# Kernel tuning notes

Hardware: AMD Instinct MI355X
Metric: run time of the kernel (lower is better)

Reference implementation:

```python
import jax, jax.numpy as jnp
import numpy as np

N_NODES = 50000
N_REL = 500
D = 128
N_EDGES = 600000


def setup_inputs() -> dict:
    key = jax.random.key(0)
    k1, k2, k3, k4, k5 = jax.random.split(key, 5)
    h = jax.random.normal(k1, (N_NODES, D), dtype=jnp.float32)
    g = jax.random.normal(k2, (N_REL, D), dtype=jnp.float32)
    row = jax.random.randint(k3, (N_EDGES,), 0, N_NODES)
    col = jax.random.randint(k4, (N_EDGES,), 0, N_NODES)
    edge_idx = jnp.stack([row, col], axis=0)  # [2, E]
    edge_type = jax.random.randint(k5, (N_EDGES,), 0, N_REL)
    return {"h": h, "g": g, "edge_idx": edge_idx, "edge_type": edge_type}


def reference(h, g, edge_idx, edge_type):
    # d = || h[row] + g[type] - h[col] ||_1 per edge  -> [E]
    row, col = edge_idx[0], edge_idx[1]
    diff = h[row] + g[edge_type] - h[col]  # [E, D] fused gather+combine
    return jnp.sum(jnp.abs(diff), axis=1)
```

## Files before the change

### kernel.cpp

```cpp
#include <hip/hip_runtime.h>
#include <hip/hip_fp16.h>


#define D 128
typedef float f32x2 __attribute__((ext_vector_type(2)));

__global__ void __launch_bounds__(256) KB_cvt(
    const float* __restrict__ h_in, unsigned int* __restrict__ h8, int n4_h,
    const float* __restrict__ g_in, unsigned int* __restrict__ g8, int n4_g)
{
    const int total = n4_h + n4_g;
    for (int i = blockIdx.x * 256 + threadIdx.x; i < total; i += gridDim.x * 256) {
        const bool isH = (i < n4_h);
        const int  j   = isH ? i : i - n4_h;
        const float4 v = isH ? reinterpret_cast<const float4*>(h_in)[j]
                             : reinterpret_cast<const float4*>(g_in)[j];
        unsigned int w = 0;
        w = __builtin_amdgcn_cvt_pk_fp8_f32(v.x, v.y, w, false);
        w = __builtin_amdgcn_cvt_pk_fp8_f32(v.z, v.w, w, true);
        (isH ? h8 : g8)[j] = w;
    }
}

__global__ void __launch_bounds__(256, 4) KB_main(
    const unsigned int* __restrict__ h8,
    const unsigned int* __restrict__ g8,
    const int* __restrict__ eidx,
    const int* __restrict__ etype,
    float* __restrict__ out,
    int E)
{
    const int grp = (blockIdx.x * 256 + (int)threadIdx.x) >> 3;
    const int sub = threadIdx.x & 7;
    const int e0  = grp * 4;
    if (e0 >= E) return;

    int r[4], c[4], t[4];
    #pragma unroll
    for (int k = 0; k < 4; ++k) {
        const int e = min(e0 + k, E - 1);
        r[k] = eidx[e];
        c[k] = eidx[E + e];
        t[k] = etype[e];
    }

    uint4 hr[4], hc[4], gw[4];
    #pragma unroll
    for (int k = 0; k < 4; ++k)
        hr[k] = *reinterpret_cast<const uint4*>(h8 + (size_t)r[k] * 32 + sub * 4);
    #pragma unroll
    for (int k = 0; k < 4; ++k)
        hc[k] = *reinterpret_cast<const uint4*>(h8 + (size_t)c[k] * 32 + sub * 4);
    #pragma unroll
    for (int k = 0; k < 4; ++k)
        gw[k] = *reinterpret_cast<const uint4*>(g8 + (size_t)t[k] * 32 + sub * 4);

    float s0 = 0.f, s1 = 0.f, s2 = 0.f, s3 = 0.f;
    #pragma unroll
    for (int k = 0; k < 4; ++k) {
        const unsigned int ha[4] = {hr[k].x, hr[k].y, hr[k].z, hr[k].w};
        const unsigned int hb[4] = {hc[k].x, hc[k].y, hc[k].z, hc[k].w};
        const unsigned int gg[4] = {gw[k].x, gw[k].y, gw[k].z, gw[k].w};
        float s = 0.f;
        #pragma unroll
        for (int j = 0; j < 4; ++j) {
            const f32x2 a0 = __builtin_amdgcn_cvt_pk_f32_fp8(ha[j], false);
            const f32x2 a1 = __builtin_amdgcn_cvt_pk_f32_fp8(ha[j], true);
            const f32x2 c0 = __builtin_amdgcn_cvt_pk_f32_fp8(hb[j], false);
            const f32x2 c1 = __builtin_amdgcn_cvt_pk_f32_fp8(hb[j], true);
            const f32x2 g0 = __builtin_amdgcn_cvt_pk_f32_fp8(gg[j], false);
            const f32x2 g1 = __builtin_amdgcn_cvt_pk_f32_fp8(gg[j], true);
            s += fabsf(a0.x + g0.x - c0.x) + fabsf(a0.y + g0.y - c0.y)
               + fabsf(a1.x + g1.x - c1.x) + fabsf(a1.y + g1.y - c1.y);
        }
        s += __shfl_xor(s, 4, 8);
        s += __shfl_xor(s, 2, 8);
        s += __shfl_xor(s, 1, 8);
        if (k == 0) s0 = s; else if (k == 1) s1 = s; else if (k == 2) s2 = s; else s3 = s;
    }

    const float v = (sub == 0) ? s0 : (sub == 1) ? s1 : (sub == 2) ? s2 : s3;
    if (sub < 4 && e0 + sub < E) out[e0 + sub] = v;
}

__global__ void __launch_bounds__(256) KB_transe_l1_f32(
    const float* __restrict__ h, const float* __restrict__ g,
    const int* __restrict__ eidx, const int* __restrict__ etype,
    float* __restrict__ out, int E)
{
    const int tid  = blockIdx.x * 256 + threadIdx.x;
    const int edge = tid >> 5;
    const int lane = threadIdx.x & 31;
    if (edge >= E) return;
    const int r = eidx[edge], c = eidx[E + edge], t = etype[edge];
    const int d = lane * 4;
    const float4 hr = *reinterpret_cast<const float4*>(h + (size_t)r * D + d);
    const float4 hc = *reinterpret_cast<const float4*>(h + (size_t)c * D + d);
    const float4 gt = *reinterpret_cast<const float4*>(g + (size_t)t * D + d);
    float s = fabsf(hr.x + gt.x - hc.x) + fabsf(hr.y + gt.y - hc.y)
            + fabsf(hr.z + gt.z - hc.z) + fabsf(hr.w + gt.w - hc.w);
    #pragma unroll
    for (int o = 16; o >= 1; o >>= 1) s += __shfl_xor(s, o, 32);
    if (lane == 0) out[edge] = s;
}

extern "C" void kernel_launch(void* const* d_in, const int* in_sizes, int n_in,
                              void* d_out, int out_size, void* d_ws, size_t ws_size,
                              hipStream_t stream) {
    const float* h     = (const float*)d_in[0];
    const float* g     = (const float*)d_in[1];
    const int*   eidx  = (const int*)d_in[2];
    const int*   etype = (const int*)d_in[3];
    float*       out   = (float*)d_out;

    const int E   = in_sizes[3];
    const int n_h = in_sizes[0];
    const int n_g = in_sizes[1];

    const size_t need = (size_t)n_h + (size_t)n_g;
    const bool ok = (n_h % 4 == 0) && (n_g % 4 == 0) && (n_h % D == 0) && (n_g % D == 0);

    if (ws_size >= need && ok) {
        unsigned int* h8 = (unsigned int*)d_ws;
        unsigned int* g8 = (unsigned int*)((char*)d_ws + (size_t)n_h);
        const int n4_h = n_h / 4, n4_g = n_g / 4;
        const int cgrid = (n4_h + n4_g + 255) / 256;
        KB_cvt<<<cgrid, 256, 0, stream>>>(h, h8, n4_h, g, g8, n4_g);

        const int groups = (E + 3) / 4;
        const long long threads = (long long)groups * 8;
        const int grid = (int)((threads + 255) / 256);
        KB_main<<<grid, 256, 0, stream>>>(h8, g8, eidx, etype, out, E);
    } else {
        const long long threads = (long long)E * 32;
        const int grid = (int)((threads + 255) / 256);
        KB_transe_l1_f32<<<grid, 256, 0, stream>>>(h, g, eidx, etype, out, E);
    }
}
```

Before: 29.33 us.

## Stage relation table in LDS with persistent 1024-thread grid-stride blocks

Copies the fp8 relation embedding table (500x128 bytes, 64KB) into shared memory once per block, and reads relation rows from LDS instead of global memory. The kernel becomes persistent: 512 blocks of 1024 threads loop over 512-edge chunks. This removes one global gather per edge, at the cost of a 64KB LDS footprint that limits occupancy to about one or two blocks per CU, plus an up-front table load in every block.

Result: slower. 31.35 us (+6.9%).

```diff
diff --git a/kernel.cpp b/kernel.cpp
--- a/kernel.cpp
+++ b/kernel.cpp
@@ -3,6 +3,7 @@
 
 
 #define D 128
+#define MAXREL 500
 typedef float f32x2 __attribute__((ext_vector_type(2)));
 
 __global__ void __launch_bounds__(256) KB_cvt(
@@ -22,65 +23,79 @@
     }
 }
 
-__global__ void __launch_bounds__(256, 4) KB_main(
+__global__ void __launch_bounds__(1024) KB_main(
     const unsigned int* __restrict__ h8,
     const unsigned int* __restrict__ g8,
     const int* __restrict__ eidx,
     const int* __restrict__ etype,
     float* __restrict__ out,
-    int E)
+    int E, int ng_u4, int niter)
 {
-    const int grp = (blockIdx.x * 256 + (int)threadIdx.x) >> 3;
+    __shared__ unsigned int gs[MAXREL * (D / 4)];
+
+    {
+        uint4* gsv = reinterpret_cast<uint4*>(gs);
+        const uint4* gv = reinterpret_cast<const uint4*>(g8);
+        for (int i = threadIdx.x; i < ng_u4; i += 1024) gsv[i] = gv[i];
+    }
+    __syncthreads();
+
+    const int grp = threadIdx.x >> 3;
     const int sub = threadIdx.x & 7;
-    const int e0  = grp * 4;
-    if (e0 >= E) return;
 
-    int r[4], c[4], t[4];
-    #pragma unroll
-    for (int k = 0; k < 4; ++k) {
-        const int e = min(e0 + k, E - 1);
-        r[k] = eidx[e];
-        c[k] = eidx[E + e];
-        t[k] = etype[e];
+    for (int it = blockIdx.x; it < niter; it += gridDim.x) {
+        const int e0 = it * 512 + grp * 4;
+        if (e0 >= E) continue;
+
+        int r[4], c[4], t[4];
+        #pragma unroll
+        for (int k = 0; k < 4; ++k) {
+            const int e = min(e0 + k, E - 1);
+            r[k] = eidx[e];
+            c[k] = eidx[E + e];
+            t[k] = etype[e];
+        }
+
+        uint4 hr[4], hc[4];
+        #pragma unroll
+        for (int k = 0; k < 4; ++k)
+            hr[k] = *reinterpret_cast<const uint4*>(h8 + (size_t)r[k] * 32 + sub * 4);
+        #pragma unroll
+        for (int k = 0; k < 4; ++k)
+            hc[k] = *reinterpret_cast<const uint4*>(h8 + (size_t)c[k] * 32 + sub * 4);
+
+        uint4 gw[4];
+        #pragma unroll
+        for (int k = 0; k < 4; ++k)
+            gw[k] = *reinterpret_cast<const uint4*>(gs + t[k] * 32 + sub * 4);
+
+        float s0 = 0.f, s1 = 0.f, s2 = 0.f, s3 = 0.f;
+        #pragma unroll
+        for (int k = 0; k < 4; ++k) {
+            const unsigned int ha[4] = {hr[k].x, hr[k].y, hr[k].z, hr[k].w};
+            const unsigned int hb[4] = {hc[k].x, hc[k].y, hc[k].z, hc[k].w};
+            const unsigned int gg[4] = {gw[k].x, gw[k].y, gw[k].z, gw[k].w};
+            float s = 0.f;
+            #pragma unroll
+            for (int j = 0; j < 4; ++j) {
+                const f32x2 a0 = __builtin_amdgcn_cvt_pk_f32_fp8(ha[j], false);
+                const f32x2 a1 = __builtin_amdgcn_cvt_pk_f32_fp8(ha[j], true);
+                const f32x2 c0 = __builtin_amdgcn_cvt_pk_f32_fp8(hb[j], false);
+                const f32x2 c1 = __builtin_amdgcn_cvt_pk_f32_fp8(hb[j], true);
+                const f32x2 g0 = __builtin_amdgcn_cvt_pk_f32_fp8(gg[j], false);
+                const f32x2 g1 = __builtin_amdgcn_cvt_pk_f32_fp8(gg[j], true);
+                s += fabsf(a0.x + g0.x - c0.x) + fabsf(a0.y + g0.y - c0.y)
+                   + fabsf(a1.x + g1.x - c1.x) + fabsf(a1.y + g1.y - c1.y);
+            }
+            s += __shfl_xor(s, 4, 8);
+            s += __shfl_xor(s, 2, 8);
+            s += __shfl_xor(s, 1, 8);
+            if (k == 0) s0 = s; else if (k == 1) s1 = s; else if (k == 2) s2 = s; else s3 = s;
+        }
+
+        const float v = (sub == 0) ? s0 : (sub == 1) ? s1 : (sub == 2) ? s2 : s3;
+        if (sub < 4 && e0 + sub < E) out[e0 + sub] = v;
     }
-
-    uint4 hr[4], hc[4], gw[4];
-    #pragma unroll
-    for (int k = 0; k < 4; ++k)
-        hr[k] = *reinterpret_cast<const uint4*>(h8 + (size_t)r[k] * 32 + sub * 4);
-    #pragma unroll
-    for (int k = 0; k < 4; ++k)
-        hc[k] = *reinterpret_cast<const uint4*>(h8 + (size_t)c[k] * 32 + sub * 4);
-    #pragma unroll
-    for (int k = 0; k < 4; ++k)
-        gw[k] = *reinterpret_cast<const uint4*>(g8 + (size_t)t[k] * 32 + sub * 4);
-
-    float s0 = 0.f, s1 = 0.f, s2 = 0.f, s3 = 0.f;
-    #pragma unroll
-    for (int k = 0; k < 4; ++k) {
-        const unsigned int ha[4] = {hr[k].x, hr[k].y, hr[k].z, hr[k].w};
-        const unsigned int hb[4] = {hc[k].x, hc[k].y, hc[k].z, hc[k].w};
-        const unsigned int gg[4] = {gw[k].x, gw[k].y, gw[k].z, gw[k].w};
-        float s = 0.f;
-        #pragma unroll
-        for (int j = 0; j < 4; ++j) {
-            const f32x2 a0 = __builtin_amdgcn_cvt_pk_f32_fp8(ha[j], false);
-            const f32x2 a1 = __builtin_amdgcn_cvt_pk_f32_fp8(ha[j], true);
-            const f32x2 c0 = __builtin_amdgcn_cvt_pk_f32_fp8(hb[j], false);
-            const f32x2 c1 = __builtin_amdgcn_cvt_pk_f32_fp8(hb[j], true);
-            const f32x2 g0 = __builtin_amdgcn_cvt_pk_f32_fp8(gg[j], false);
-            const f32x2 g1 = __builtin_amdgcn_cvt_pk_f32_fp8(gg[j], true);
-            s += fabsf(a0.x + g0.x - c0.x) + fabsf(a0.y + g0.y - c0.y)
-               + fabsf(a1.x + g1.x - c1.x) + fabsf(a1.y + g1.y - c1.y);
-        }
-        s += __shfl_xor(s, 4, 8);
-        s += __shfl_xor(s, 2, 8);
-        s += __shfl_xor(s, 1, 8);
-        if (k == 0) s0 = s; else if (k == 1) s1 = s; else if (k == 2) s2 = s; else s3 = s;
-    }
-
-    const float v = (sub == 0) ? s0 : (sub == 1) ? s1 : (sub == 2) ? s2 : s3;
-    if (sub < 4 && e0 + sub < E) out[e0 + sub] = v;
 }
 
 __global__ void __launch_bounds__(256) KB_transe_l1_f32(
@@ -118,7 +133,7 @@
     const int n_g = in_sizes[1];
 
     const size_t need = (size_t)n_h + (size_t)n_g;
-    const bool ok = (n_h % 4 == 0) && (n_g % 4 == 0) && (n_h % D == 0) && (n_g % D == 0);
+    const bool ok = (n_g / D) <= MAXREL && (n_g % 16 == 0) && (n_h % D == 0);
 
     if (ws_size >= need && ok) {
         unsigned int* h8 = (unsigned int*)d_ws;
@@ -127,10 +142,8 @@
         const int cgrid = (n4_h + n4_g + 255) / 256;
         KB_cvt<<<cgrid, 256, 0, stream>>>(h, h8, n4_h, g, g8, n4_g);
 
-        const int groups = (E + 3) / 4;
-        const long long threads = (long long)groups * 8;
-        const int grid = (int)((threads + 255) / 256);
-        KB_main<<<grid, 256, 0, stream>>>(h8, g8, eidx, etype, out, E);
+        const int niter = (E + 511) / 512;
+        KB_main<<<512, 1024, 0, stream>>>(h8, g8, eidx, etype, out, E, n_g / 16, niter);
     } else {
         const long long threads = (long long)E * 32;
         const int grid = (int)((threads + 255) / 256);
```
